# Kernel optimization log

Measured on AMD Instinct MI355X. Metric: run time of the kernel, lower is better.

Reference implementation:

```python
import jax, jax.numpy as jnp
import numpy as np

N, E, G = 50000, 800000, 64
IN, HID, H, C, OUT = 4, 128, 2, 64, 7  # HID = heads*C = 128
EPS = 1e-5
NEG_SLOPE = 0.2


def setup_inputs() -> dict:
    key = jax.random.key(0)
    ks = jax.random.split(key, 24)
    rn = lambda k, shape, s=0.1: (jax.random.normal(k, shape, jnp.float32) * s)
    inp = {
        "x": jax.random.normal(ks[0], (N, IN), jnp.float32),
        "edge_index": jax.random.randint(ks[1], (2, E), 0, N, jnp.int64),
        "batch": jnp.sort(jax.random.randint(ks[2], (N,), 0, G, jnp.int64)),
        # GATv2 layer 1: lin_l (source), lin_r (target), attention vector, bias
        "Wl1": rn(ks[3], (IN, HID)), "Wr1": rn(ks[4], (IN, HID)),
        "att1": rn(ks[5], (H, C)), "b1": rn(ks[6], (HID,)),
        "g1": jnp.ones((HID,), jnp.float32), "be1": jnp.zeros((HID,), jnp.float32),
        # GATv2 layer 2
        "Wl2": rn(ks[7], (HID, HID)), "Wr2": rn(ks[8], (HID, HID)),
        "att2": rn(ks[9], (H, C)), "b2": rn(ks[10], (HID,)),
        "g2": jnp.ones((HID,), jnp.float32), "be2": jnp.zeros((HID,), jnp.float32),
        # MLP head
        "W3": rn(ks[11], (HID, C)), "b3": rn(ks[12], (C,)),
        "W4": rn(ks[13], (C, OUT)), "b4": rn(ks[14], (OUT,)),
    }
    return inp


def gatv2_conv(x, src, dst, Wl, Wr, att, bias):
    """PyG GATv2Conv, heads=H, concat=True, self-loops already in (src,dst)."""
    n = x.shape[0]
    xl = (x @ Wl).reshape(n, H, C)  # source-side transform
    xr = (x @ Wr).reshape(n, H, C)  # target-side transform
    m = xl[src] + xr[dst]                                   # [E', H, C]
    e = jnp.einsum('ehc,hc->eh', jax.nn.leaky_relu(m, NEG_SLOPE), att)
    # segment softmax over edges sharing a destination node
    emax = jax.ops.segment_max(e, dst, num_segments=n)
    p = jnp.exp(e - emax[dst])
    denom = jax.ops.segment_sum(p, dst, num_segments=n)
    alpha = p / denom[dst]                                  # [E', H]
    out = jax.ops.segment_sum(alpha[..., None] * xl[src], dst, num_segments=n)
    return out.reshape(n, H * C) + bias


def batchnorm(x, gamma, beta):
    mu = jnp.mean(x, axis=0)
    var = jnp.mean(jnp.square(x - mu), axis=0)  # biased var (torch train norm)
    return gamma * (x - mu) * jax.lax.rsqrt(var + EPS) + beta


def reference(x, edge_index, batch, Wl1, Wr1, att1, b1, g1, be1,
              Wl2, Wr2, att2, b2, g2, be2, W3, b3, W4, b4):
    n = x.shape[0]
    loops = jnp.arange(n, dtype=edge_index.dtype)
    src = jnp.concatenate([edge_index[0], loops])
    dst = jnp.concatenate([edge_index[1], loops])

    h = jax.nn.relu(batchnorm(gatv2_conv(x, src, dst, Wl1, Wr1, att1, b1), g1, be1))
    h = jax.nn.relu(batchnorm(gatv2_conv(h, src, dst, Wl2, Wr2, att2, b2), g2, be2))

    # global mean pool over graphs
    sums = jax.ops.segment_sum(h, batch, num_segments=G)
    cnts = jax.ops.segment_sum(jnp.ones((n, 1), h.dtype), batch, num_segments=G)
    pooled = sums / jnp.maximum(cnts, 1.0)

    out = jax.nn.relu(pooled @ W3 + b3)
    return out @ W4 + b4
```

## Files before the change

kernel.cpp:

```cpp
#include <hip/hip_runtime.h>
#include <hip/hip_bf16.h>

typedef __hip_bfloat16 bf16;
typedef unsigned short u16;
typedef unsigned int u32;
typedef long long i64;
typedef short bf16x8 __attribute__((ext_vector_type(8)));
typedef float f32x4 __attribute__((ext_vector_type(4)));

#define N_NODES 50000
#define E_EDGES 800000
#define G_GRAPHS 64
#define HID 128
#define OUT_F 7
#define EPSBN 1e-5f
#define NEG 0.2f
#define NB_G 2048
#define SCAN_B 196
#define PB_NODES 32
#define XP 136
#define NXF 25000
#define NEB 3125

__device__ __forceinline__ float b2f(bf16 v) { return __bfloat162float(v); }
__device__ __forceinline__ float ldf(const void* p, int i, int fm) {
    return fm ? ((const float*)p)[i] : b2f(((const bf16*)p)[i]);
}
__device__ __forceinline__ int ldi(const void* p, i64 i, int im) {
    return im ? (int)((const i64*)p)[i] : ((const int*)p)[i];
}
__device__ __forceinline__ void stf(void* p, int i, int fm, float v) {
    if (fm) ((float*)p)[i] = v; else ((bf16*)p)[i] = __float2bfloat16(v);
}
__device__ __forceinline__ float bl(u32 u) { return __uint_as_float(u << 16); }
__device__ __forceinline__ float bh(u32 u) { return __uint_as_float(u & 0xFFFF0000u); }

template <int CTRL>
__device__ __forceinline__ float dpp_add(float t) {
    int v = __builtin_amdgcn_update_dpp(0, __float_as_int(t), CTRL, 0xF, 0xF, true);
    return t + __int_as_float(v);
}

__global__ void k_init(const void* __restrict__ x, const void* __restrict__ ei,
                       int* __restrict__ flags,
                       float* __restrict__ z1, int n1, float* __restrict__ z2, int n2) {
    int t = threadIdx.x;
    if (blockIdx.x == 0) {
        __shared__ int sh[2];
        if (t == 0) { sh[0] = 0; sh[1] = 1; }
        __syncthreads();
        const u16* xb = (const u16*)x;
        int huge = 0;
        for (int i = t; i < 1024; i += 256) {
            int e = (xb[i] >> 7) & 0xFF;
            if (e >= 0x90) huge = 1;
        }
        if (huge) atomicOr(&sh[0], 1);
        const u32* eb = (const u32*)ei;
        int nz = 0;
        for (int i = t; i < 512; i += 256)
            if (eb[2 * i + 1] != 0) nz = 1;
        if (nz) atomicAnd(&sh[1], 0);
        __syncthreads();
        if (t == 0) { flags[0] = sh[0]; flags[1] = sh[1]; }
    } else {
        int i = (blockIdx.x - 1) * 256 + t;
        int stride = (gridDim.x - 1) * 256;
        for (; i < n1 + n2; i += stride) {
            if (i < n1) z1[i] = 0.0f;
            else z2[i - n1] = 0.0f;
        }
    }
}

__global__ __launch_bounds__(256) void k_prepdeg(
    const void* __restrict__ x, const void* __restrict__ Wl, const void* __restrict__ Wr,
    const void* __restrict__ Wl2, const void* __restrict__ Wr2,
    const void* __restrict__ ei, const int* __restrict__ flags,
    bf16* __restrict__ xl, bf16* __restrict__ xr, bf16* __restrict__ WT,
    int* __restrict__ deg) {
    int b = blockIdx.x;
    if (b < NXF) {
        int fm = flags[0];
        int idx = b * 256 + threadIdx.x;
        int n = idx >> 7, j = idx & 127;
        float a = 0.f, bb = 0.f;
#pragma unroll
        for (int k = 0; k < 4; k++) {
            float xv = ldf(x, n * 4 + k, fm);
            a += xv * ldf(Wl, k * HID + j, fm);
            bb += xv * ldf(Wr, k * HID + j, fm);
        }
        xl[idx] = __float2bfloat16(a);
        xr[idx] = __float2bfloat16(bb);
    } else if (b < NXF + 128) {
        int fm = flags[0];
        int idx = (b - NXF) * 256 + threadIdx.x;
        int mat = idx >> 14, r = idx & 16383, j = r >> 7, k = r & 127;
        const void* W = mat ? Wr2 : Wl2;
        WT[idx] = __float2bfloat16(ldf(W, k * HID + j, fm));
    } else {
        int im = flags[1];
        int e = (b - NXF - 128) * 256 + threadIdx.x;
        if (e < E_EDGES) {
            int d = ldi(ei, (i64)E_EDGES + e, im);
            atomicAdd(&deg[d], 1);
        }
    }
}

__global__ void k_scan1(const int* __restrict__ deg, int* __restrict__ bsum) {
    __shared__ int s[256];
    int t = threadIdx.x, i = blockIdx.x * 256 + t;
    s[t] = (i < N_NODES) ? deg[i] : 0;
    __syncthreads();
    for (int off = 128; off > 0; off >>= 1) {
        if (t < off) s[t] += s[t + off];
        __syncthreads();
    }
    if (t == 0) bsum[blockIdx.x] = s[0];
}

__global__ void k_scan2(int* __restrict__ bsum) {
    __shared__ int s[256];
    int t = threadIdx.x;
    int orig = (t < SCAN_B) ? bsum[t] : 0;
    s[t] = orig;
    __syncthreads();
    for (int off = 1; off < 256; off <<= 1) {
        int v = (t >= off) ? s[t - off] : 0;
        __syncthreads();
        s[t] += v;
        __syncthreads();
    }
    if (t < SCAN_B) bsum[t] = s[t] - orig;
}

__global__ void k_scan3(const int* __restrict__ deg, const int* __restrict__ bsum,
                        int* __restrict__ rowptr, int* __restrict__ cursor) {
    __shared__ int s[256];
    int t = threadIdx.x, i = blockIdx.x * 256 + t;
    int v = (i < N_NODES) ? deg[i] : 0;
    s[t] = v;
    __syncthreads();
    for (int off = 1; off < 256; off <<= 1) {
        int a = (t >= off) ? s[t - off] : 0;
        __syncthreads();
        s[t] += a;
        __syncthreads();
    }
    int excl = s[t] - v + bsum[blockIdx.x];
    if (i < N_NODES) { rowptr[i] = excl; cursor[i] = excl; }
    if (i == N_NODES - 1) rowptr[N_NODES] = excl + v;
}

__global__ void k_fill(const void* __restrict__ ei, const int* __restrict__ flags,
                       int* __restrict__ cursor, int* __restrict__ csr) {
    int im = flags[1];
    int e = blockIdx.x * 256 + threadIdx.x;
    if (e >= E_EDGES) return;
    int src = ldi(ei, e, im);
    int d   = ldi(ei, (i64)E_EDGES + e, im);
    int pos = atomicAdd(&cursor[d], 1);
    csr[pos] = src;
}

__global__ __launch_bounds__(256) void k_gather(
    const bf16* __restrict__ XLp, const bf16* __restrict__ XRp,
    const void* __restrict__ att, const void* __restrict__ bias,
    const int* __restrict__ rowptr, const int* __restrict__ csr,
    const int* __restrict__ flags,
    float* __restrict__ A, float* __restrict__ partial) {
    __shared__ float ls[128], lq[128];
    int t = threadIdx.x;
    if (t < 128) { ls[t] = 0.f; lq[t] = 0.f; }
    __syncthreads();
    int fm = flags[0];
    int lane = t & 63, waveid = t >> 6;
    int half = lane >> 5;
    int headq = (lane >> 4) & 1;
    int c16 = lane & 15;
    int cbase = headq * 64 + c16 * 4;
    const u32* XLw = (const u32*)XLp;
    const u32* XRw = (const u32*)XRp;
    u32 coff = (u32)(cbase >> 1);
    float a0 = ldf(att, cbase + 0, fm), a1 = ldf(att, cbase + 1, fm);
    float a2 = ldf(att, cbase + 2, fm), a3 = ldf(att, cbase + 3, fm);
    float bb0 = ldf(bias, cbase + 0, fm), bb1 = ldf(bias, cbase + 1, fm);
    float bb2 = ldf(bias, cbase + 2, fm), bb3 = ldf(bias, cbase + 3, fm);
    float s0 = 0, s1 = 0, s2 = 0, s3 = 0, q0 = 0, q1 = 0, q2 = 0, q3 = 0;

    for (int d = blockIdx.x * 4 + waveid; d < N_NODES; d += NB_G * 4) {
        int rp = rowptr[d];
        int deg = rowptr[d + 1] - rp;
        int count = deg + 1;
        u32 roff = ((u32)d << 6) + coff;
        u32 r01 = XRw[roff], r23 = XRw[roff + 1];
        float xr0 = bl(r01), xr1 = bh(r01), xr2 = bl(r23), xr3 = bh(r23);
        float acc0 = 0, acc1 = 0, acc2 = 0, acc3 = 0, den = 0;
        int sA = d; if (half < deg) sA = csr[rp + half];
        int sB = d; if (2 + half < deg) sB = csr[rp + 2 + half];
        u32 offA = ((u32)sA << 6) + coff;
        u32 a01 = XLw[offA], a23 = XLw[offA + 1];
        u32 offB = ((u32)sB << 6) + coff;
        u32 b01 = XLw[offB], b23 = XLw[offB + 1];
        int sC = d; if (4 + half < deg) sC = csr[rp + 4 + half];
        int sD = d; if (6 + half < deg) sD = csr[rp + 6 + half];
        for (int i = 0; i < count; i += 4) {
            u32 offC = ((u32)sC << 6) + coff;
            u32 n01 = XLw[offC], n23 = XLw[offC + 1];
            u32 offD = ((u32)sD << 6) + coff;
            u32 m01 = XLw[offD], m23 = XLw[offD + 1];
            int eE = i + 8 + half, eF = i + 10 + half;
            int sE = d; if (eE < deg) sE = csr[rp + eE];
            int sF = d; if (eF < deg) sF = csr[rp + eF];
            {
                float x0 = bl(a01), x1 = bh(a01), x2 = bl(a23), x3 = bh(a23);
                float m0 = x0 + xr0, m1 = x1 + xr1, m2 = x2 + xr2, m3 = x3 + xr3;
                m0 = fmaxf(m0, NEG * m0);
                m1 = fmaxf(m1, NEG * m1);
                m2 = fmaxf(m2, NEG * m2);
                m3 = fmaxf(m3, NEG * m3);
                float tt = fmaf(m0, a0, fmaf(m1, a1, fmaf(m2, a2, m3 * a3)));
                tt = dpp_add<0xB1>(tt);
                tt = dpp_add<0x4E>(tt);
                tt = dpp_add<0x141>(tt);
                tt = dpp_add<0x140>(tt);
                float p = __expf(tt);
                if (i + half >= count) p = 0.f;
                den += p;
                acc0 = fmaf(p, x0, acc0); acc1 = fmaf(p, x1, acc1);
                acc2 = fmaf(p, x2, acc2); acc3 = fmaf(p, x3, acc3);
            }
            {
                float x0 = bl(b01), x1 = bh(b01), x2 = bl(b23), x3 = bh(b23);
                float m0 = x0 + xr0, m1 = x1 + xr1, m2 = x2 + xr2, m3 = x3 + xr3;
                m0 = fmaxf(m0, NEG * m0);
                m1 = fmaxf(m1, NEG * m1);
                m2 = fmaxf(m2, NEG * m2);
                m3 = fmaxf(m3, NEG * m3);
                float tt = fmaf(m0, a0, fmaf(m1, a1, fmaf(m2, a2, m3 * a3)));
                tt = dpp_add<0xB1>(tt);
                tt = dpp_add<0x4E>(tt);
                tt = dpp_add<0x141>(tt);
                tt = dpp_add<0x140>(tt);
                float p = __expf(tt);
                if (i + 2 + half >= count) p = 0.f;
                den += p;
                acc0 = fmaf(p, x0, acc0); acc1 = fmaf(p, x1, acc1);
                acc2 = fmaf(p, x2, acc2); acc3 = fmaf(p, x3, acc3);
            }
            a01 = n01; a23 = n23; b01 = m01; b23 = m23;
            sC = sE; sD = sF;
        }
        acc0 += __shfl_xor(acc0, 32, 64);
        acc1 += __shfl_xor(acc1, 32, 64);
        acc2 += __shfl_xor(acc2, 32, 64);
        acc3 += __shfl_xor(acc3, 32, 64);
        den  += __shfl_xor(den, 32, 64);
        if (lane < 32) {
            float inv = __builtin_amdgcn_rcpf(den);
            float v0 = fmaf(acc0, inv, bb0);
            float v1 = fmaf(acc1, inv, bb1);
            float v2 = fmaf(acc2, inv, bb2);
            float v3 = fmaf(acc3, inv, bb3);
            *(float4*)(A + (size_t)d * HID + cbase) = make_float4(v0, v1, v2, v3);
            s0 += v0; s1 += v1; s2 += v2; s3 += v3;
            q0 += v0 * v0; q1 += v1 * v1; q2 += v2 * v2; q3 += v3 * v3;
        }
    }
    if (lane < 32) {
        atomicAdd(&ls[cbase + 0], s0); atomicAdd(&ls[cbase + 1], s1);
        atomicAdd(&ls[cbase + 2], s2); atomicAdd(&ls[cbase + 3], s3);
        atomicAdd(&lq[cbase + 0], q0); atomicAdd(&lq[cbase + 1], q1);
        atomicAdd(&lq[cbase + 2], q2); atomicAdd(&lq[cbase + 3], q3);
    }
    __syncthreads();
    if (t < 128) partial[blockIdx.x * 256 + t] = ls[t];
    else if (t < 256) partial[blockIdx.x * 256 + t] = lq[t - 128];
}

__global__ __launch_bounds__(256) void k_bnred(const float* __restrict__ partial,
                                               float* __restrict__ sums) {
    int t = threadIdx.x;
    float acc = 0.f;
    for (int b = blockIdx.x; b < NB_G; b += 256) acc += partial[b * 256 + t];
    unsafeAtomicAdd(&sums[t], acc);
}

__device__ __forceinline__ void bn_params_lds(
    const float* __restrict__ sums, const void* __restrict__ g, const void* __restrict__ be,
    int fm, float* scs, float* shs, int t) {
    if (t < 128) {
        float mu = sums[t] * (1.0f / N_NODES);
        float var = sums[t + 128] * (1.0f / N_NODES) - mu * mu;
        float sc = ldf(g, t, fm) * rsqrtf(var + EPSBN);
        scs[t] = sc;
        shs[t] = ldf(be, t, fm) - mu * sc;
    }
}

__global__ __launch_bounds__(256) void k_xform2(
    const float* __restrict__ A, const float* __restrict__ sums,
    const void* __restrict__ g, const void* __restrict__ be,
    const int* __restrict__ flags,
    const bf16* __restrict__ WT, bf16* __restrict__ XLp, bf16* __restrict__ XRp) {
    __shared__ __align__(16) bf16 at[32 * XP];
    __shared__ __align__(16) bf16 wt[128 * XP];
    __shared__ float scs[128], shs[128];
    int t = threadIdx.x;
    int fm = flags[0];
    bn_params_lds(sums, g, be, fm, scs, shs, t);
    __syncthreads();
    int n0 = blockIdx.x * 32;
    int mat = blockIdx.y;
    bf16* outp = mat ? XRp : XLp;
    const bf16* wsrc = WT + mat * HID * HID;
    {
        int m = t >> 3, kb = (t & 7) * 16;
        int n = n0 + m;
        float vals[16];
        if (n < N_NODES) {
            const float4* src = (const float4*)(A + (size_t)n * HID + kb);
#pragma unroll
            for (int i = 0; i < 4; i++) {
                float4 f = src[i];
                vals[4 * i + 0] = f.x; vals[4 * i + 1] = f.y;
                vals[4 * i + 2] = f.z; vals[4 * i + 3] = f.w;
            }
#pragma unroll
            for (int i = 0; i < 16; i++) {
                float v = fmaf(vals[i], scs[kb + i], shs[kb + i]);
                vals[i] = v > 0.f ? v : 0.f;
            }
        } else {
#pragma unroll
            for (int i = 0; i < 16; i++) vals[i] = 0.f;
        }
        u32* dst = (u32*)(at + m * XP + kb);
#pragma unroll
        for (int i = 0; i < 8; i++) {
            u32 lo = __bfloat16_as_ushort(__float2bfloat16(vals[2 * i]));
            u32 hi = __bfloat16_as_ushort(__float2bfloat16(vals[2 * i + 1]));
            dst[i] = lo | (hi << 16);
        }
    }
    {
        int j = t >> 1, kh = (t & 1) * 64;
        const uint4* s4 = (const uint4*)(wsrc + j * HID + kh);
        uint4* d4 = (uint4*)(wt + j * XP + kh);
#pragma unroll
        for (int i = 0; i < 8; i++) d4[i] = s4[i];
    }
    __syncthreads();
    int w = t >> 6, lane = t & 63;
    int mtile = w & 1, ng = (w >> 1) * 4;
    int l15 = lane & 15, quad = lane >> 4;
    f32x4 acc[4] = {{0,0,0,0},{0,0,0,0},{0,0,0,0},{0,0,0,0}};
#pragma unroll
    for (int ks = 0; ks < 4; ks++) {
        int k0 = ks * 32 + quad * 8;
        bf16x8 af = *(const bf16x8*)(at + (mtile * 16 + l15) * XP + k0);
#pragma unroll
        for (int nt = 0; nt < 4; nt++) {
            bf16x8 bfr = *(const bf16x8*)(wt + ((ng + nt) * 16 + l15) * XP + k0);
            acc[nt] = __builtin_amdgcn_mfma_f32_16x16x32_bf16(af, bfr, acc[nt], 0, 0, 0);
        }
    }
#pragma unroll
    for (int nt = 0; nt < 4; nt++) {
        int j = (ng + nt) * 16 + l15;
#pragma unroll
        for (int r = 0; r < 4; r++) {
            int n = n0 + mtile * 16 + quad * 4 + r;
            if (n < N_NODES) outp[(size_t)n * HID + j] = __float2bfloat16(acc[nt][r]);
        }
    }
}

__global__ __launch_bounds__(256) void k_pool(
    const float* __restrict__ A, const float* __restrict__ sums,
    const void* __restrict__ g, const void* __restrict__ be,
    const void* __restrict__ batch, const int* __restrict__ flags,
    float* __restrict__ pools, float* __restrict__ cnt) {
    __shared__ float scs[128], shs[128];
    int t = threadIdx.x;
    int fm = flags[0], im = flags[1];
    bn_params_lds(sums, g, be, fm, scs, shs, t);
    __syncthreads();
    int j = t & 127, sub = t >> 7;
    int nstart = blockIdx.x * PB_NODES + sub;
    int nend = min(blockIdx.x * PB_NODES + PB_NODES, N_NODES);
    float sc = scs[j], sh = shs[j];
    float acc = 0.f; int run = 0; int gcur = -1;
    for (int n = nstart; n < nend; n += 2) {
        int gg = ldi(batch, n, im);
        if (gg != gcur) {
            if (run > 0) {
                unsafeAtomicAdd(&pools[gcur * HID + j], acc);
                if (j == 0) unsafeAtomicAdd(&cnt[gcur], (float)run);
            }
            gcur = gg; acc = 0.f; run = 0;
        }
        float v = fmaf(A[(size_t)n * HID + j], sc, sh);
        acc += v > 0.f ? v : 0.f;
        run++;
    }
    if (run > 0) {
        unsafeAtomicAdd(&pools[gcur * HID + j], acc);
        if (j == 0) unsafeAtomicAdd(&cnt[gcur], (float)run);
    }
}

__global__ __launch_bounds__(64) void k_head(
    const float* __restrict__ pools, const float* __restrict__ cnt,
    const void* __restrict__ W3, const void* __restrict__ b3,
    const void* __restrict__ W4, const void* __restrict__ b4,
    const int* __restrict__ flags, void* __restrict__ out) {
    __shared__ float p[HID];
    __shared__ float z[64];
    int fm = flags[0];
    int g = blockIdx.x, t = threadIdx.x;
    float inv = 1.0f / fmaxf(cnt[g], 1.0f);
    p[t]      = pools[g * HID + t] * inv;
    p[t + 64] = pools[g * HID + 64 + t] * inv;
    __syncthreads();
    float acc = ldf(b3, t, fm);
    for (int j = 0; j < HID; j++) acc += p[j] * ldf(W3, j * 64 + t, fm);
    z[t] = acc > 0.f ? acc : 0.f;
    __syncthreads();
    if (t < OUT_F) {
        float o = ldf(b4, t, fm);
        for (int c = 0; c < 64; c++) o += z[c] * ldf(W4, c * OUT_F + t, fm);
        stf(out, g * OUT_F + t, fm, o);
    }
}

extern "C" void kernel_launch(void* const* d_in, const int* in_sizes, int n_in,
                              void* d_out, int out_size, void* d_ws, size_t ws_size,
                              hipStream_t stream) {
    const void* x    = d_in[0];
    const void* ei   = d_in[1];
    const void* batch= d_in[2];
    const void* Wl1  = d_in[3];
    const void* Wr1  = d_in[4];
    const void* att1 = d_in[5];
    const void* b1   = d_in[6];
    const void* g1   = d_in[7];
    const void* be1  = d_in[8];
    const void* Wl2  = d_in[9];
    const void* Wr2  = d_in[10];
    const void* att2 = d_in[11];
    const void* b2   = d_in[12];
    const void* g2   = d_in[13];
    const void* be2  = d_in[14];
    const void* W3   = d_in[15];
    const void* b3   = d_in[16];
    const void* W4   = d_in[17];
    const void* b4   = d_in[18];

    int*   flags  = (int*)d_ws;
    float* A      = (float*)((char*)d_ws + 64);
    int*   deg    = (int*)A;
    int*   rowptr = (int*)(A + (size_t)N_NODES * HID);
    int*   csr    = rowptr + (N_NODES + 1);
    float* partial= (float*)(csr + E_EDGES);
    int*   cursor = (int*)partial;
    float* pools  = partial + (size_t)NB_G * 256;
    float* cnt    = pools + G_GRAPHS * HID;
    float* bnS1   = cnt + G_GRAPHS;
    float* bnS2   = bnS1 + 256;
    int*   bsum   = (int*)(bnS2 + 256);
    bf16*  WT     = (bf16*)(bsum + 256);
    bf16*  XL     = WT + 2 * HID * HID;
    bf16*  XR     = XL + (size_t)N_NODES * HID;

    const size_t NEEDED = 64
        + sizeof(float) * (size_t)N_NODES * HID
        + sizeof(int) * ((size_t)N_NODES + 1 + E_EDGES)
        + sizeof(float) * ((size_t)NB_G * 256 + G_GRAPHS * HID + G_GRAPHS + 512 + 256)
        + sizeof(bf16) * (2 * HID * HID + 2 * (size_t)N_NODES * HID);
    if (ws_size < NEEDED) return;

    const int zlen2 = G_GRAPHS * HID + G_GRAPHS + 512;

    k_init<<<129, 256, 0, stream>>>(x, ei, flags, (float*)deg, N_NODES, pools, zlen2);
    k_prepdeg<<<NXF + 128 + NEB, 256, 0, stream>>>(x, Wl1, Wr1, Wl2, Wr2, ei, flags, XL, XR, WT, deg);

    k_scan1<<<SCAN_B, 256, 0, stream>>>(deg, bsum);
    k_scan2<<<1, 256, 0, stream>>>(bsum);
    k_scan3<<<SCAN_B, 256, 0, stream>>>(deg, bsum, rowptr, cursor);
    k_fill<<<NEB, 256, 0, stream>>>(ei, flags, cursor, csr);

    k_gather<<<NB_G, 256, 0, stream>>>(XL, XR, att1, b1, rowptr, csr, flags, A, partial);
    k_bnred<<<256, 256, 0, stream>>>(partial, bnS1);

    k_xform2<<<dim3((N_NODES + 31) / 32, 2), 256, 0, stream>>>(A, bnS1, g1, be1, flags, WT, XL, XR);
    k_gather<<<NB_G, 256, 0, stream>>>(XL, XR, att2, b2, rowptr, csr, flags, A, partial);
    k_bnred<<<256, 256, 0, stream>>>(partial, bnS2);

    k_pool<<<(N_NODES + PB_NODES - 1) / PB_NODES, 256, 0, stream>>>(
        A, bnS2, g2, be2, batch, flags, pools, cnt);
    k_head<<<G_GRAPHS, 64, 0, stream>>>(pools, cnt, W3, b3, W4, b4, flags, d_out);
}
```

Before: 395.5 us.

## Make layer-2 transform persistent with weights held in registers

The second-layer linear transform kernel now runs a fixed grid of persistent blocks that loop over 16-node tiles. Each block loads its weight fragments for both Wl and Wr into registers once instead of staging a full weight matrix through LDS per 32-node block. Each activation tile is normalized and read once, then used for both output matrices, which halves the reads of A and removes the per-block weight reload. The cost is higher register pressure (64 VGPRs of weight fragments) and two barriers per tile, with less parallelism per tile.

```diff
diff --git a/kernel.cpp b/kernel.cpp
--- a/kernel.cpp
+++ b/kernel.cpp
@@ -21,6 +21,8 @@
 #define XP 136
 #define NXF 25000
 #define NEB 3125
+#define NB_X 1024
+#define NTILES 3125
 
 __device__ __forceinline__ float b2f(bf16 v) { return __bfloat162float(v); }
 __device__ __forceinline__ float ldf(const void* p, int i, int fm) {
@@ -305,76 +307,67 @@
     const void* __restrict__ g, const void* __restrict__ be,
     const int* __restrict__ flags,
     const bf16* __restrict__ WT, bf16* __restrict__ XLp, bf16* __restrict__ XRp) {
-    __shared__ __align__(16) bf16 at[32 * XP];
-    __shared__ __align__(16) bf16 wt[128 * XP];
+    __shared__ __align__(16) bf16 at[16 * XP];
     __shared__ float scs[128], shs[128];
     int t = threadIdx.x;
     int fm = flags[0];
     bn_params_lds(sums, g, be, fm, scs, shs, t);
-    __syncthreads();
-    int n0 = blockIdx.x * 32;
-    int mat = blockIdx.y;
+    int lane = t & 63, w = t >> 6;
+    int mat = w & 1, half = w >> 1;
     bf16* outp = mat ? XRp : XLp;
-    const bf16* wsrc = WT + mat * HID * HID;
+    int l15 = lane & 15, quad = lane >> 4;
+    bf16x8 bfrag[4][4];
     {
-        int m = t >> 3, kb = (t & 7) * 16;
-        int n = n0 + m;
-        float vals[16];
-        if (n < N_NODES) {
-            const float4* src = (const float4*)(A + (size_t)n * HID + kb);
+        const bf16* wbase = WT + mat * HID * HID;
+#pragma unroll
+        for (int nt = 0; nt < 4; nt++)
+#pragma unroll
+            for (int ks = 0; ks < 4; ks++)
+                bfrag[nt][ks] = *(const bf16x8*)(
+                    wbase + ((half * 4 + nt) * 16 + l15) * HID + ks * 32 + quad * 8);
+    }
+    __syncthreads();
+    int sn = t >> 4, sc = (t & 15) * 8;
+    for (int tile = blockIdx.x; tile < NTILES; tile += NB_X) {
+        int n0 = tile * 16;
+        {
+            const float4* src = (const float4*)(A + (size_t)(n0 + sn) * HID + sc);
+            float4 f0 = src[0], f1 = src[1];
+            float v[8] = {f0.x, f0.y, f0.z, f0.w, f1.x, f1.y, f1.z, f1.w};
+            u32 pk[4];
+#pragma unroll
+            for (int i = 0; i < 8; i++) {
+                float vv = fmaf(v[i], scs[sc + i], shs[sc + i]);
+                v[i] = vv > 0.f ? vv : 0.f;
+            }
 #pragma unroll
             for (int i = 0; i < 4; i++) {
-                float4 f = src[i];
-                vals[4 * i + 0] = f.x; vals[4 * i + 1] = f.y;
-                vals[4 * i + 2] = f.z; vals[4 * i + 3] = f.w;
-            }
-#pragma unroll
-            for (int i = 0; i < 16; i++) {
-                float v = fmaf(vals[i], scs[kb + i], shs[kb + i]);
-                vals[i] = v > 0.f ? v : 0.f;
-            }
-        } else {
-#pragma unroll
-            for (int i = 0; i < 16; i++) vals[i] = 0.f;
-        }
-        u32* dst = (u32*)(at + m * XP + kb);
-#pragma unroll
-        for (int i = 0; i < 8; i++) {
-            u32 lo = __bfloat16_as_ushort(__float2bfloat16(vals[2 * i]));
-            u32 hi = __bfloat16_as_ushort(__float2bfloat16(vals[2 * i + 1]));
-            dst[i] = lo | (hi << 16);
-        }
-    }
-    {
-        int j = t >> 1, kh = (t & 1) * 64;
-        const uint4* s4 = (const uint4*)(wsrc + j * HID + kh);
-        uint4* d4 = (uint4*)(wt + j * XP + kh);
-#pragma unroll
-        for (int i = 0; i < 8; i++) d4[i] = s4[i];
-    }
-    __syncthreads();
-    int w = t >> 6, lane = t & 63;
-    int mtile = w & 1, ng = (w >> 1) * 4;
-    int l15 = lane & 15, quad = lane >> 4;
-    f32x4 acc[4] = {{0,0,0,0},{0,0,0,0},{0,0,0,0},{0,0,0,0}};
-#pragma unroll
-    for (int ks = 0; ks < 4; ks++) {
-        int k0 = ks * 32 + quad * 8;
-        bf16x8 af = *(const bf16x8*)(at + (mtile * 16 + l15) * XP + k0);
+                u32 lo = __bfloat16_as_ushort(__float2bfloat16(v[2 * i]));
+                u32 hi = __bfloat16_as_ushort(__float2bfloat16(v[2 * i + 1]));
+                pk[i] = lo | (hi << 16);
+            }
+            u32* dst = (u32*)(at + sn * XP + sc);
+            dst[0] = pk[0]; dst[1] = pk[1]; dst[2] = pk[2]; dst[3] = pk[3];
+        }
+        __syncthreads();
+        f32x4 acc[4] = {{0,0,0,0},{0,0,0,0},{0,0,0,0},{0,0,0,0}};
+#pragma unroll
+        for (int ks = 0; ks < 4; ks++) {
+            bf16x8 af = *(const bf16x8*)(at + l15 * XP + ks * 32 + quad * 8);
+#pragma unroll
+            for (int nt = 0; nt < 4; nt++)
+                acc[nt] = __builtin_amdgcn_mfma_f32_16x16x32_bf16(af, bfrag[nt][ks], acc[nt], 0, 0, 0);
+        }
 #pragma unroll
         for (int nt = 0; nt < 4; nt++) {
-            bf16x8 bfr = *(const bf16x8*)(wt + ((ng + nt) * 16 + l15) * XP + k0);
-            acc[nt] = __builtin_amdgcn_mfma_f32_16x16x32_bf16(af, bfr, acc[nt], 0, 0, 0);
-        }
-    }
-#pragma unroll
-    for (int nt = 0; nt < 4; nt++) {
-        int j = (ng + nt) * 16 + l15;
-#pragma unroll
-        for (int r = 0; r < 4; r++) {
-            int n = n0 + mtile * 16 + quad * 4 + r;
-            if (n < N_NODES) outp[(size_t)n * HID + j] = __float2bfloat16(acc[nt][r]);
-        }
+            int j = half * 64 + nt * 16 + l15;
+#pragma unroll
+            for (int r = 0; r < 4; r++) {
+                int n = n0 + quad * 4 + r;
+                outp[(size_t)n * HID + j] = __float2bfloat16(acc[nt][r]);
+            }
+        }
+        __syncthreads();
     }
 }
 
@@ -495,7 +488,7 @@
     k_gather<<<NB_G, 256, 0, stream>>>(XL, XR, att1, b1, rowptr, csr, flags, A, partial);
     k_bnred<<<256, 256, 0, stream>>>(partial, bnS1);
 
-    k_xform2<<<dim3((N_NODES + 31) / 32, 2), 256, 0, stream>>>(A, bnS1, g1, be1, flags, WT, XL, XR);
+    k_xform2<<<NB_X, 256, 0, stream>>>(A, bnS1, g1, be1, flags, WT, XL, XR);
     k_gather<<<NB_G, 256, 0, stream>>>(XL, XR, att2, b2, rowptr, csr, flags, A, partial);
     k_bnred<<<256, 256, 0, stream>>>(partial, bnS2);
 
```

Result: faster. 382.5 us (-3.3%).
